# Kernel optimization log

Measured on AMD Instinct MI355X. Metric: run time of the kernel, lower is better.

## Reference

```python
import jax, jax.numpy as jnp
import numpy as np

D = 128          # embed_dim
NB = 30          # hardcoded neighbor count in neighbor_encoder
STEPS = 4        # process_steps
NSYM = 200000    # num_symbols (pad idx = NSYM)
B = 4096         # query batch
FEW = 5          # support pairs


def setup_inputs() -> dict:
    key = jax.random.key(0)
    ks = jax.random.split(key, 32)
    g = lambda i, shape, s=0.02: jax.random.normal(ks[i], shape, dtype=jnp.float32) * s
    inp = {}
    # embedding tables (row NSYM is padding, zeros)
    inp['emb'] = g(0, (NSYM + 1, D), 0.1).at[NSYM].set(0.0)
    inp['emb_var'] = g(1, (NSYM + 1, D), 0.1).at[NSYM].set(0.0)
    # neighbor attention (mean path)
    inp['nW'], inp['nWb'] = g(2, (D, 2 * D)), jnp.zeros((D,), jnp.float32)
    inp['nu'], inp['nub'] = g(3, (1, D)), jnp.zeros((1,), jnp.float32)
    # neighbor attention (var path)
    inp['nvW'], inp['nvWb'] = g(4, (D, 2 * D)), jnp.zeros((D,), jnp.float32)
    inp['nvu'], inp['nvub'] = g(5, (1, D)), jnp.zeros((1,), jnp.float32)
    # SupportEncoder: d_model=2D, d_inner=4D
    inp['p1W'], inp['p1b'] = g(6, (4 * D, 2 * D)), jnp.zeros((4 * D,), jnp.float32)
    inp['p2W'], inp['p2b'] = g(7, (2 * D, 4 * D)), jnp.zeros((2 * D,), jnp.float32)
    inp['ln_a'], inp['ln_b'] = jnp.ones((2 * D,), jnp.float32), jnp.zeros((2 * D,), jnp.float32)
    # QueryEncoder LSTMCell: input 2D, hidden 4D (torch gate order i,f,g,o)
    inp['Wih'], inp['Whh'] = g(8, (16 * D, 2 * D)), g(9, (16 * D, 4 * D))
    inp['bih'], inp['bhh'] = jnp.zeros((16 * D,), jnp.float32), jnp.zeros((16 * D,), jnp.float32)
    # connections: (..., 0)=relation idx, (..., 1)=entity idx
    inp['q_left'] = jax.random.randint(ks[10], (B, NB, 2), 0, NSYM, dtype=jnp.int32)
    inp['q_right'] = jax.random.randint(ks[11], (B, NB, 2), 0, NSYM, dtype=jnp.int32)
    inp['s_left'] = jax.random.randint(ks[12], (FEW, NB, 2), 0, NSYM, dtype=jnp.int32)
    inp['s_right'] = jax.random.randint(ks[13], (FEW, NB, 2), 0, NSYM, dtype=jnp.int32)
    return inp


def _layer_norm(z, a, b, eps=0.001):
    # faithful to torch: std with Bessel correction (ddof=1)
    mu = jnp.mean(z, axis=-1, keepdims=True)
    sigma = jnp.std(z, axis=-1, keepdims=True, ddof=1)
    return (z - mu) / (sigma + eps) * a + b


def reference(emb, emb_var, nW, nWb, nu, nub, nvW, nvWb, nvu, nvub,
              p1W, p1b, p2W, p2b, ln_a, ln_b, Wih, Whh, bih, bhh,
              q_left, q_right, s_left, s_right):

    def neighbor_encoder(conn):
        rel, ent = conn[..., 0], conn[..., 1]
        rel_e, ent_e = emb[rel], emb[ent]                      # [N, NB, D]
        cat = jnp.concatenate([rel_e, ent_e], axis=-1)         # [N, NB, 2D]
        a = jnp.tanh(cat @ nW.T + nWb) @ nu.T + nub            # [N, NB, 1]
        att = jax.nn.softmax(a[..., 0], axis=1)                # softmax over neighbors
        out = jnp.einsum('nk,nkd->nd', att, ent_e)
        rel_v, ent_v = emb_var[rel], emb_var[ent]
        catv = jnp.concatenate([rel_v, ent_v], axis=-1)
        av = jnp.tanh(catv @ nvW.T + nvWb) @ nvu.T + nvub
        attv = jax.nn.softmax(av[..., 0], axis=1)
        out_v = jnp.einsum('nk,nkd->nd', attv, ent_e)          # torch quirk: pools ent_embeds
        return jnp.tanh(out), jnp.tanh(out_v)

    def support_encoder(x):
        h = jax.nn.relu(x @ p1W.T + p1b) @ p2W.T + p2b
        return _layer_norm(h + x, ln_a, ln_b)

    def lstm_cell(x, h, c):
        gates = x @ Wih.T + bih + h @ Whh.T + bhh
        i, f, g_, o = jnp.split(gates, 4, axis=-1)
        c = jax.nn.sigmoid(f) * c + jax.nn.sigmoid(i) * jnp.tanh(g_)
        return jax.nn.sigmoid(o) * jnp.tanh(c), c

    def query_encoder(support, query):
        n = query.shape[0]
        h_r = jnp.zeros((n, 4 * D), query.dtype)
        c = jnp.zeros((n, 4 * D), query.dtype)
        h = query
        for _ in range(STEPS):
            h_r_, c = lstm_cell(query, h_r, c)
            h = query + h_r_[:, :2 * D]
            attn = jax.nn.softmax(h @ support.T, axis=1)
            r = attn @ support
            h_r = jnp.concatenate([h, r], axis=1)
        return h

    ql, qlv = neighbor_encoder(q_left)
    qr, qrv = neighbor_encoder(q_right)
    sl, slv = neighbor_encoder(s_left)
    sr, srv = neighbor_encoder(s_right)

    query = jnp.concatenate([ql, qr], axis=-1)       # [B, 2D]
    query_v = jnp.concatenate([qlv, qrv], axis=-1)
    support = jnp.concatenate([sl, sr], axis=-1)     # [FEW, 2D]
    support_v = jnp.concatenate([slv, srv], axis=-1)

    def match(q, s):
        s_g = support_encoder(s)
        q_g = support_encoder(q)
        q_f = query_encoder(s_g, q_g)
        s_mean = jnp.mean(s_g, axis=0, keepdims=True)  # [1, 2D]
        return (q_f @ s_mean.T)[:, 0]                  # [B]

    score = match(query, support)
    score_var = match(query_v, support_v)
    return jnp.stack([score, score_var])               # [2, B]
```

## Files before the change

kernel.cpp:

```cpp
#include <hip/hip_runtime.h>
#include <math.h>

#define DD    128
#define TWOD  256
#define FOURD 512
#define NBN   30
#define BQ    4096
#define FEWN  5
#define NSYM  200000
#define KTOT  768
#define NGATE 1024
#define ULIVE 256
#define TOTU  (2 * BQ + 2 * FEWN)
#define UPB   4
#define PSTR  136

typedef short bf16x8 __attribute__((ext_vector_type(8)));
typedef float f32x4 __attribute__((ext_vector_type(4)));

__device__ __forceinline__ float sigmoidf_(float x) { return 1.0f / (1.0f + expf(-x)); }

__device__ __forceinline__ float ftanh(float x) {
    float e = __expf(2.0f * x);
    return 1.0f - 2.0f / (e + 1.0f);
}

__device__ __forceinline__ unsigned short f2bf(float f) {
    unsigned int u = __float_as_uint(f);
    unsigned int r = (u + 0x7fffu + ((u >> 16) & 1u)) >> 16;
    return (unsigned short)r;
}

__device__ __forceinline__ float bf2f(unsigned short s) {
    return __uint_as_float(((unsigned int)s) << 16);
}

__device__ __forceinline__ bf16x8 pack8(float4 a, float4 b) {
    union { bf16x8 v; unsigned int u[4]; } r;
    r.u[0] = ((__float_as_uint(a.x) + 0x8000u) >> 16) | ((__float_as_uint(a.y) + 0x8000u) & 0xffff0000u);
    r.u[1] = ((__float_as_uint(a.z) + 0x8000u) >> 16) | ((__float_as_uint(a.w) + 0x8000u) & 0xffff0000u);
    r.u[2] = ((__float_as_uint(b.x) + 0x8000u) >> 16) | ((__float_as_uint(b.y) + 0x8000u) & 0xffff0000u);
    r.u[3] = ((__float_as_uint(b.z) + 0x8000u) >> 16) | ((__float_as_uint(b.w) + 0x8000u) & 0xffff0000u);
    return r.v;
}

__device__ __forceinline__ void gload_lds16(const void* g, void* l) {
    __builtin_amdgcn_global_load_lds((const __attribute__((address_space(1))) unsigned int*)g,
                                     (__attribute__((address_space(3))) unsigned int*)l,
                                     16, 0, 0);
}

__global__ __launch_bounds__(256) void k_prep(
    const float* __restrict__ Wih, const float* __restrict__ Whh,
    const float* __restrict__ bih, const float* __restrict__ bhh,
    const float* __restrict__ p1W, const float* __restrict__ p2W,
    const float* __restrict__ nW, const float* __restrict__ nvW,
    unsigned short* __restrict__ Wbf, float* __restrict__ biasR,
    float* __restrict__ p1WT, float* __restrict__ p2WT,
    unsigned short* __restrict__ Nbf)
{
    int idx = blockIdx.x * 256 + threadIdx.x;
    int stride = gridDim.x * 256;
    for (int i = idx; i < NGATE * KTOT; i += stride) {
        int n = i / KTOT, k = i - n * KTOT;
        int blk = n >> 6, rem = n & 63;
        int g = rem >> 4, ul = rem & 15;
        int u = blk * 16 + ul;
        int srcrow = g * 512 + u;
        float v = (k < TWOD) ? Wih[srcrow * TWOD + k] : Whh[srcrow * FOURD + (k - TWOD)];
        Wbf[i] = f2bf(v);
    }
    for (int n = idx; n < NGATE; n += stride) {
        int blk = n >> 6, rem = n & 63;
        int g = rem >> 4, ul = rem & 15;
        int u = blk * 16 + ul;
        int srcrow = g * 512 + u;
        biasR[n] = bih[srcrow] + bhh[srcrow];
    }
    for (int i = idx; i < FOURD * TWOD; i += stride) {
        int o = i / TWOD, j = i % TWOD;
        p1WT[j * FOURD + o] = p1W[o * TWOD + j];
    }
    for (int i = idx; i < TWOD * FOURD; i += stride) {
        int o = i / FOURD, j = i % FOURD;
        p2WT[j * TWOD + o] = p2W[o * FOURD + j];
    }
    for (int i = idx; i < 2 * DD * TWOD; i += stride) {
        float v = (i < DD * TWOD) ? nW[i] : nvW[i - DD * TWOD];
        Nbf[i] = f2bf(v);
    }
}

__global__ __launch_bounds__(256, 2) void k_neighbor_v4(
    const float* __restrict__ emb, const float* __restrict__ emb_var,
    const unsigned short* __restrict__ Nbf,
    const float* __restrict__ nWb, const float* __restrict__ nu,
    const float* __restrict__ nvWb, const float* __restrict__ nvu,
    const int* __restrict__ q_left, const int* __restrict__ q_right,
    const int* __restrict__ s_left, const int* __restrict__ s_right,
    float* __restrict__ query, float* __restrict__ support)
{
    const int tid  = threadIdx.x;
    const int wave = tid >> 6, lane = tid & 63;
    const int quad = lane >> 4, m15 = lane & 15;
    const int pw   = wave >> 1;
    const int wn   = wave & 1;
    const int u0   = blockIdx.x * UPB;

    __shared__ __align__(16) unsigned short Sg[4 * 32 * PSTR];
    __shared__ int   sidxL[UPB][64];
    __shared__ float aP[2][2][32];
    __shared__ float attL[2][32];

    {
        int un = tid >> 6, i = tid & 63;
        int uu_ = u0 + un; if (uu_ >= TOTU) uu_ = TOTU - 1;
        const int* conn;
        if (uu_ < BQ)                 conn = q_left  + uu_ * (NBN * 2);
        else if (uu_ < 2 * BQ)        conn = q_right + (uu_ - BQ) * (NBN * 2);
        else if (uu_ < 2 * BQ + FEWN) conn = s_left  + (uu_ - 2 * BQ) * (NBN * 2);
        else                          conn = s_right + (uu_ - 2 * BQ - FEWN) * (NBN * 2);
        sidxL[un][i] = (i < NBN * 2) ? conn[i] : NSYM;
    }

    const unsigned short* Bw = Nbf + (size_t)pw * DD * TWOD;
    const float* Wb = pw ? nvWb : nWb;
    const float* uu = pw ? nvu  : nu;
    bf16x8 Bf[4][8];
    float nb[4], un_[4];
#pragma unroll
    for (int t = 0; t < 4; ++t) {
        int n = wn * 64 + t * 16 + m15;
#pragma unroll
        for (int kt = 0; kt < 8; ++kt)
            Bf[t][kt] = *(const bf16x8*)(Bw + n * TWOD + kt * 32 + quad * 8);
        nb[t] = Wb[n];
        un_[t] = uu[n];
    }
    __syncthreads();

    for (int r = 0; r < UPB; ++r) {
        const int uidx = u0 + r;

        {
            const int g = wave;
            const float* table = (g < 2) ? emb : emb_var;
            const int side = g & 1;
            const int colf = (lane & 15) * 8;
            const int rsub = lane >> 4;
#pragma unroll
            for (int i = 0; i < 8; ++i) {
                int row = i * 4 + rsub;
                int sym = sidxL[r][2 * row + side];
                const float* src = table + (size_t)sym * DD + colf;
                float4 x0 = *(const float4*)src;
                float4 x1 = *(const float4*)(src + 4);
                *(bf16x8*)&Sg[(g * 32 + row) * PSTR + colf] = pack8(x0, x1);
            }
        }
        __syncthreads();

        const int pg = pw ? 2 : 0;
        f32x4 acc[2][4] = {};
#pragma unroll
        for (int kt = 0; kt < 8; ++kt) {
            const int g = (kt < 4) ? pg : pg + 1;
            const int coff = (kt & 3) * 32 + quad * 8;
            bf16x8 fa[2];
#pragma unroll
            for (int mt = 0; mt < 2; ++mt)
                fa[mt] = *(const bf16x8*)&Sg[(g * 32 + mt * 16 + m15) * PSTR + coff];
#pragma unroll
            for (int mt = 0; mt < 2; ++mt)
#pragma unroll
                for (int nt = 0; nt < 4; ++nt)
                    acc[mt][nt] = __builtin_amdgcn_mfma_f32_16x16x32_bf16(fa[mt], Bf[nt][kt], acc[mt][nt], 0, 0, 0);
        }

        {
            float part[2][4];
#pragma unroll
            for (int mt = 0; mt < 2; ++mt)
#pragma unroll
                for (int rr = 0; rr < 4; ++rr) {
                    float s = 0.f;
#pragma unroll
                    for (int nt = 0; nt < 4; ++nt)
                        s += un_[nt] * ftanh(acc[mt][nt][rr] + nb[nt]);
                    part[mt][rr] = s;
                }
#pragma unroll
            for (int off = 1; off < 16; off <<= 1)
#pragma unroll
                for (int mt = 0; mt < 2; ++mt)
#pragma unroll
                    for (int rr = 0; rr < 4; ++rr)
                        part[mt][rr] += __shfl_xor(part[mt][rr], off, 64);
            if (m15 == 0) {
#pragma unroll
                for (int mt = 0; mt < 2; ++mt)
#pragma unroll
                    for (int rr = 0; rr < 4; ++rr)
                        aP[pw][wn][mt * 16 + quad * 4 + rr] = part[mt][rr];
            }
        }
        __syncthreads();

        if ((wave & 1) == 0 && lane < 32) {
            const int p = wave >> 1;
            float sc = (lane < NBN) ? aP[p][0][lane] + aP[p][1][lane] : -1e30f;
            float mx = sc;
#pragma unroll
            for (int off = 1; off < 32; off <<= 1) mx = fmaxf(mx, __shfl_xor(mx, off, 64));
            float e = (lane < NBN) ? __expf(sc - mx) : 0.f;
            float sum = e;
#pragma unroll
            for (int off = 1; off < 32; off <<= 1) sum += __shfl_xor(sum, off, 64);
            attL[p][lane] = e / sum;
        }
        __syncthreads();

        {
            const int p = tid >> 7;
            const int d = tid & 127;
            float pool = 0.f;
#pragma unroll
            for (int k = 0; k < NBN; ++k)
                pool += attL[p][k] * bf2f(Sg[(32 + k) * PSTR + d]);
            if (uidx < TOTU) {
                float* dst;
                if (uidx < BQ)                 dst = query   + ((size_t)p * BQ + uidx) * TWOD;
                else if (uidx < 2 * BQ)        dst = query   + ((size_t)p * BQ + (uidx - BQ)) * TWOD + DD;
                else if (uidx < 2 * BQ + FEWN) dst = support + ((size_t)p * FEWN + (uidx - 2 * BQ)) * TWOD;
                else                           dst = support + ((size_t)p * FEWN + (uidx - 2 * BQ - FEWN)) * TWOD + DD;
                dst[d] = ftanh(pool);
            }
        }
        __syncthreads();
    }
}

template <int RPB>
__global__ __launch_bounds__(256) void k_supenc(
    const float* __restrict__ xin, float* __restrict__ xout,
    unsigned short* __restrict__ abf,
    const float* __restrict__ p1WT, const float* __restrict__ p1b,
    const float* __restrict__ p2WT, const float* __restrict__ p2b,
    const float* __restrict__ ln_a, const float* __restrict__ ln_b)
{
    const int tid = threadIdx.x;
    const int r0 = blockIdx.x * RPB;
    __shared__ float X[RPB][TWOD];
    __shared__ float H1[RPB][FOURD];
    __shared__ float red[4][RPB][2];
    __shared__ float muv[RPB], sgv[RPB];

    for (int idx = tid; idx < RPB * TWOD; idx += 256) {
        int r = idx >> 8, j = idx & 255;
        X[r][j] = xin[(size_t)(r0 + r) * TWOD + j];
    }
    __syncthreads();

    {
        float acc[RPB][2] = {};
        for (int j = 0; j < TWOD; j += 4) {
            float w0[4], w1[4];
#pragma unroll
            for (int jj = 0; jj < 4; ++jj) {
                w0[jj] = p1WT[(j + jj) * FOURD + tid];
                w1[jj] = p1WT[(j + jj) * FOURD + tid + 256];
            }
#pragma unroll
            for (int r = 0; r < RPB; ++r) {
                float x[4] __attribute__((aligned(16)));
                *(float4*)x = *(const float4*)&X[r][j];
#pragma unroll
                for (int jj = 0; jj < 4; ++jj) {
                    acc[r][0] += x[jj] * w0[jj];
                    acc[r][1] += x[jj] * w1[jj];
                }
            }
        }
        float b0 = p1b[tid], b1 = p1b[tid + 256];
#pragma unroll
        for (int r = 0; r < RPB; ++r) {
            H1[r][tid]       = fmaxf(acc[r][0] + b0, 0.f);
            H1[r][tid + 256] = fmaxf(acc[r][1] + b1, 0.f);
        }
    }
    __syncthreads();

    float z[RPB];
    {
        float acc[RPB] = {};
        for (int j = 0; j < FOURD; j += 4) {
            float w[4];
#pragma unroll
            for (int jj = 0; jj < 4; ++jj) w[jj] = p2WT[(j + jj) * TWOD + tid];
#pragma unroll
            for (int r = 0; r < RPB; ++r) {
                float h[4] __attribute__((aligned(16)));
                *(float4*)h = *(const float4*)&H1[r][j];
#pragma unroll
                for (int jj = 0; jj < 4; ++jj) acc[r] += h[jj] * w[jj];
            }
        }
        float b = p2b[tid];
#pragma unroll
        for (int r = 0; r < RPB; ++r) z[r] = acc[r] + b + X[r][tid];
    }
    {
        float s[RPB], ss[RPB];
#pragma unroll
        for (int r = 0; r < RPB; ++r) { s[r] = z[r]; ss[r] = z[r] * z[r]; }
#pragma unroll
        for (int off = 1; off < 64; off <<= 1)
#pragma unroll
            for (int r = 0; r < RPB; ++r) {
                s[r]  += __shfl_xor(s[r],  off, 64);
                ss[r] += __shfl_xor(ss[r], off, 64);
            }
        const int wv = tid >> 6, lane = tid & 63;
        if (lane == 0) {
#pragma unroll
            for (int r = 0; r < RPB; ++r) { red[wv][r][0] = s[r]; red[wv][r][1] = ss[r]; }
        }
        __syncthreads();
        if (tid < RPB) {
            float st  = red[0][tid][0] + red[1][tid][0] + red[2][tid][0] + red[3][tid][0];
            float sst = red[0][tid][1] + red[1][tid][1] + red[2][tid][1] + red[3][tid][1];
            float mu  = st / (float)TWOD;
            float var = fmaxf((sst - (float)TWOD * mu * mu) / ((float)TWOD - 1.f), 0.f);
            muv[tid] = mu; sgv[tid] = sqrtf(var);
        }
        __syncthreads();
    }
#pragma unroll
    for (int r = 0; r < RPB; ++r) {
        float o = (z[r] - muv[r]) / (sgv[r] + 1e-3f) * ln_a[tid] + ln_b[tid];
        xout[(size_t)(r0 + r) * TWOD + tid] = o;
        if (abf) abf[(size_t)(r0 + r) * KTOT + tid] = f2bf(o);
    }
}

__global__ __launch_bounds__(256) void k_lstm_mfma(
    const unsigned short* __restrict__ Abf,
    const unsigned short* __restrict__ Wbf,
    const float* __restrict__ biasR,
    float* __restrict__ cst, float* __restrict__ hbuf)
{
    __shared__ __align__(16) unsigned short As[128 * 32];
    __shared__ __align__(16) unsigned short Bs[128 * 32];
    const int tid  = threadIdx.x;
    const int wave = tid >> 6, lane = tid & 63;
    const int quad = lane >> 4, m15 = lane & 15;
    const int m0 = blockIdx.x * 128;
    const int n0 = blockIdx.y * 128;
    const int wm = wave >> 1, wn = wave & 1;
    const int lrow = lane >> 2, lslot = lane & 3;

    f32x4 acc[4][4] = {};

    for (int kt = 0; kt < KTOT / 32; ++kt) {
        const int k0 = kt * 32;
        __syncthreads();
#pragma unroll
        for (int t = 0; t < 2; ++t) {
            int c = wave * 2 + t;
            int row = c * 16 + lrow;
            int kg = lslot ^ ((row >> 1) & 3);
            gload_lds16(Abf + (size_t)(m0 + row) * KTOT + k0 + kg * 8, As + c * 512);
            gload_lds16(Wbf + (size_t)(n0 + row) * KTOT + k0 + kg * 8, Bs + c * 512);
        }
        __syncthreads();

        bf16x8 fa[4], fb[4];
#pragma unroll
        for (int mi = 0; mi < 4; ++mi) {
            int ra = wm * 64 + mi * 16 + m15;
            int sa = quad ^ ((ra >> 1) & 3);
            fa[mi] = *(const bf16x8*)(As + ra * 32 + sa * 8);
            int rb = wn * 64 + mi * 16 + m15;
            int sb = quad ^ ((rb >> 1) & 3);
            fb[mi] = *(const bf16x8*)(Bs + rb * 32 + sb * 8);
        }
#pragma unroll
        for (int mi = 0; mi < 4; ++mi)
#pragma unroll
            for (int ni = 0; ni < 4; ++ni)
                acc[mi][ni] = __builtin_amdgcn_mfma_f32_16x16x32_bf16(fa[mi], fb[ni], acc[mi][ni], 0, 0, 0);
    }

    const int u = ((n0 + wn * 64) >> 2) + m15;
    float bg[4];
#pragma unroll
    for (int g = 0; g < 4; ++g) bg[g] = biasR[n0 + wn * 64 + g * 16 + m15];
#pragma unroll
    for (int mi = 0; mi < 4; ++mi) {
#pragma unroll
        for (int r = 0; r < 4; ++r) {
            int gm = m0 + wm * 64 + mi * 16 + quad * 4 + r;
            size_t cidx = (size_t)gm * ULIVE + u;
            float pi = acc[mi][0][r] + bg[0];
            float pf = acc[mi][1][r] + bg[1];
            float pg = acc[mi][2][r] + bg[2];
            float po = acc[mi][3][r] + bg[3];
            float cn = sigmoidf_(pf) * cst[cidx] + sigmoidf_(pi) * tanhf(pg);
            cst[cidx]  = cn;
            hbuf[cidx] = sigmoidf_(po) * tanhf(cn);
        }
    }
}

__global__ __launch_bounds__(256) void k_lstm_attn(
    const float* __restrict__ qg, const float* __restrict__ hbuf,
    const float* __restrict__ sg, unsigned short* __restrict__ Abf,
    float* __restrict__ hfin)
{
    const int tid = threadIdx.x;
    const int p   = blockIdx.y;
    const int wv = tid >> 6, lane = tid & 63;
    __shared__ float sgl[FEWN][TWOD];
    for (int idx = tid; idx < FEWN * TWOD; idx += 256)
        sgl[idx >> 8][idx & 255] = sg[p * FEWN * TWOD + idx];
    __syncthreads();
    const int j0 = lane * 4;
    for (int rr = 0; rr < 8; ++rr) {
        int row = blockIdx.x * 32 + wv * 8 + rr;
        size_t g = (size_t)p * BQ + row;
        float4 q4 = *(const float4*)(qg + g * TWOD + j0);
        float4 t4 = *(const float4*)(hbuf + g * ULIVE + j0);
        float h[4] __attribute__((aligned(16))) = {q4.x + t4.x, q4.y + t4.y, q4.z + t4.z, q4.w + t4.w};
        float sv[FEWN][4] __attribute__((aligned(16)));
        float pa[FEWN];
#pragma unroll
        for (int f = 0; f < FEWN; ++f) {
            *(float4*)sv[f] = *(const float4*)&sgl[f][j0];
            pa[f] = h[0] * sv[f][0] + h[1] * sv[f][1] + h[2] * sv[f][2] + h[3] * sv[f][3];
        }
#pragma unroll
        for (int off = 1; off < 64; off <<= 1)
#pragma unroll
            for (int f = 0; f < FEWN; ++f) pa[f] += __shfl_xor(pa[f], off, 64);
        float mx = pa[0];
#pragma unroll
        for (int f = 1; f < FEWN; ++f) mx = fmaxf(mx, pa[f]);
        float sum = 0.f, e[FEWN];
#pragma unroll
        for (int f = 0; f < FEWN; ++f) { e[f] = expf(pa[f] - mx); sum += e[f]; }
        float inv = 1.f / sum;
        float r4[4] __attribute__((aligned(16))) = {0.f, 0.f, 0.f, 0.f};
#pragma unroll
        for (int f = 0; f < FEWN; ++f) {
            float a = e[f] * inv;
#pragma unroll
            for (int q = 0; q < 4; ++q) r4[q] += a * sv[f][q];
        }
        unsigned short tb[4] __attribute__((aligned(8)));
#pragma unroll
        for (int q = 0; q < 4; ++q) tb[q] = f2bf(h[q]);
        *(uint2*)(Abf + g * KTOT + TWOD + j0) = *(uint2*)tb;
#pragma unroll
        for (int q = 0; q < 4; ++q) tb[q] = f2bf(r4[q]);
        *(uint2*)(Abf + g * KTOT + FOURD + j0) = *(uint2*)tb;
        *(float4*)(hfin + g * TWOD + j0) = *(float4*)h;
    }
}

__global__ __launch_bounds__(256) void k_score(
    const float* __restrict__ hfin, const float* __restrict__ sg, float* __restrict__ out)
{
    const int tid = threadIdx.x;
    const int p   = blockIdx.y;
    __shared__ float sm[TWOD];
    if (tid < TWOD) {
        const float* s = sg + p * FEWN * TWOD + tid;
        sm[tid] = (s[0] + s[TWOD] + s[2 * TWOD] + s[3 * TWOD] + s[4 * TWOD]) / 5.0f;
    }
    __syncthreads();
    const int wv = tid >> 6, lane = tid & 63;
    const int j0 = lane * 4;
    for (int rr = 0; rr < 8; ++rr) {
        int row = blockIdx.x * 32 + wv * 8 + rr;
        const float* h = hfin + ((size_t)p * BQ + row) * TWOD + j0;
        float4 h4 = *(const float4*)h;
        float4 s4 = *(const float4*)&sm[j0];
        float pv = h4.x * s4.x + h4.y * s4.y + h4.z * s4.z + h4.w * s4.w;
#pragma unroll
        for (int off = 1; off < 64; off <<= 1) pv += __shfl_xor(pv, off, 64);
        if (lane == 0) out[p * BQ + row] = pv;
    }
}

extern "C" void kernel_launch(void* const* d_in, const int* in_sizes, int n_in,
                              void* d_out, int out_size, void* d_ws, size_t ws_size,
                              hipStream_t stream)
{
    const float* emb     = (const float*)d_in[0];
    const float* emb_var = (const float*)d_in[1];
    const float* nW      = (const float*)d_in[2];
    const float* nWb     = (const float*)d_in[3];
    const float* nu      = (const float*)d_in[4];
    const float* nub     = (const float*)d_in[5];
    const float* nvW     = (const float*)d_in[6];
    const float* nvWb    = (const float*)d_in[7];
    const float* nvu     = (const float*)d_in[8];
    const float* nvub    = (const float*)d_in[9];
    const float* p1W     = (const float*)d_in[10];
    const float* p1b     = (const float*)d_in[11];
    const float* p2W     = (const float*)d_in[12];
    const float* p2b     = (const float*)d_in[13];
    const float* ln_a    = (const float*)d_in[14];
    const float* ln_b    = (const float*)d_in[15];
    const float* Wih     = (const float*)d_in[16];
    const float* Whh     = (const float*)d_in[17];
    const float* bih     = (const float*)d_in[18];
    const float* bhh     = (const float*)d_in[19];
    const int* q_left    = (const int*)d_in[20];
    const int* q_right   = (const int*)d_in[21];
    const int* s_left    = (const int*)d_in[22];
    const int* s_right   = (const int*)d_in[23];

    float* ws = (float*)d_ws;
    size_t o = 0;
    float* p1WT     = ws + o; o += FOURD * TWOD;
    float* p2WT     = ws + o; o += FOURD * TWOD;
    float* biasR    = ws + o; o += NGATE;
    float* query    = ws + o; o += (size_t)2 * BQ * TWOD;
    float* supportB = ws + o; o += 2 * FEWN * TWOD;
    float* qg       = ws + o; o += (size_t)2 * BQ * TWOD;
    float* sg       = ws + o; o += 2 * FEWN * TWOD;
    float* cst      = ws + o; o += (size_t)2 * BQ * ULIVE;
    float* hbuf     = ws + o; o += (size_t)2 * BQ * ULIVE;
    unsigned short* Wbf = (unsigned short*)(ws + o); o += (size_t)NGATE * KTOT / 2;
    unsigned short* Abf = (unsigned short*)(ws + o); o += (size_t)2 * BQ * KTOT / 2;
    unsigned short* Nbf = (unsigned short*)(ws + o); o += (size_t)2 * DD * TWOD / 2;
    float* hfin     = query;

    hipMemsetAsync(cst, 0, (size_t)2 * BQ * ULIVE * sizeof(float), stream);
    hipMemsetAsync(Abf, 0, (size_t)2 * BQ * KTOT * sizeof(unsigned short), stream);

    k_prep<<<dim3(1024), dim3(256), 0, stream>>>(Wih, Whh, bih, bhh, p1W, p2W, nW, nvW,
                                                 Wbf, biasR, p1WT, p2WT, Nbf);
    k_neighbor_v4<<<dim3((TOTU + UPB - 1) / UPB), dim3(256), 0, stream>>>(
        emb, emb_var, Nbf, nWb, nu, nvWb, nvu,
        q_left, q_right, s_left, s_right, query, supportB);
    k_supenc<8><<<dim3(2 * BQ / 8), dim3(256), 0, stream>>>(query, qg, Abf, p1WT, p1b, p2WT, p2b, ln_a, ln_b);
    k_supenc<1><<<dim3(2 * FEWN), dim3(256), 0, stream>>>(supportB, sg, (unsigned short*)nullptr,
                                                          p1WT, p1b, p2WT, p2b, ln_a, ln_b);
    for (int s = 0; s < 4; ++s) {
        k_lstm_mfma<<<dim3(2 * BQ / 128, NGATE / 128), dim3(256), 0, stream>>>(Abf, Wbf, biasR, cst, hbuf);
        k_lstm_attn<<<dim3(BQ / 32, 2), dim3(256), 0, stream>>>(qg, hbuf, sg, Abf, hfin);
    }
    k_score<<<dim3(BQ / 32, 2), dim3(256), 0, stream>>>(hfin, sg, (float*)d_out);
}
```

Before: 607.6 us.

## Gather neighbor embeddings straight to LDS in fp32; skip zero hidden-state K in first LSTM step

```diff
diff --git a/kernel.cpp b/kernel.cpp
--- a/kernel.cpp
+++ b/kernel.cpp
@@ -13,7 +13,6 @@
 #define ULIVE 256
 #define TOTU  (2 * BQ + 2 * FEWN)
 #define UPB   4
-#define PSTR  136
 
 typedef short bf16x8 __attribute__((ext_vector_type(8)));
 typedef float f32x4 __attribute__((ext_vector_type(4)));
@@ -29,10 +28,6 @@
     unsigned int u = __float_as_uint(f);
     unsigned int r = (u + 0x7fffu + ((u >> 16) & 1u)) >> 16;
     return (unsigned short)r;
-}
-
-__device__ __forceinline__ float bf2f(unsigned short s) {
-    return __uint_as_float(((unsigned int)s) << 16);
 }
 
 __device__ __forceinline__ bf16x8 pack8(float4 a, float4 b) {
@@ -91,7 +86,7 @@
     }
 }
 
-__global__ __launch_bounds__(256, 2) void k_neighbor_v4(
+__global__ __launch_bounds__(256, 2) void k_neighbor_v5(
     const float* __restrict__ emb, const float* __restrict__ emb_var,
     const unsigned short* __restrict__ Nbf,
     const float* __restrict__ nWb, const float* __restrict__ nu,
@@ -107,7 +102,7 @@
     const int wn   = wave & 1;
     const int u0   = blockIdx.x * UPB;
 
-    __shared__ __align__(16) unsigned short Sg[4 * 32 * PSTR];
+    __shared__ __align__(16) float Sgf[4 * 32 * DD];
     __shared__ int   sidxL[UPB][64];
     __shared__ float aP[2][2][32];
     __shared__ float attL[2][32];
@@ -146,16 +141,14 @@
             const int g = wave;
             const float* table = (g < 2) ? emb : emb_var;
             const int side = g & 1;
-            const int colf = (lane & 15) * 8;
-            const int rsub = lane >> 4;
-#pragma unroll
-            for (int i = 0; i < 8; ++i) {
-                int row = i * 4 + rsub;
-                int sym = sidxL[r][2 * row + side];
-                const float* src = table + (size_t)sym * DD + colf;
-                float4 x0 = *(const float4*)src;
-                float4 x1 = *(const float4*)(src + 4);
-                *(bf16x8*)&Sg[(g * 32 + row) * PSTR + colf] = pack8(x0, x1);
+            const int rl = lane >> 5;
+            const int cb = lane & 31;
+#pragma unroll
+            for (int i = 0; i < 16; ++i) {
+                const int row = 2 * i + rl;
+                const int sym = sidxL[r][2 * row + side];
+                const float* src = table + (size_t)sym * DD + ((cb ^ (row & 7)) << 2);
+                gload_lds16(src, &Sgf[(g * 32 + 2 * i) * DD]);
             }
         }
         __syncthreads();
@@ -165,11 +158,17 @@
 #pragma unroll
         for (int kt = 0; kt < 8; ++kt) {
             const int g = (kt < 4) ? pg : pg + 1;
-            const int coff = (kt & 3) * 32 + quad * 8;
+            const int cb0 = (kt & 3) * 8 + quad * 2;
             bf16x8 fa[2];
 #pragma unroll
-            for (int mt = 0; mt < 2; ++mt)
-                fa[mt] = *(const bf16x8*)&Sg[(g * 32 + mt * 16 + m15) * PSTR + coff];
+            for (int mt = 0; mt < 2; ++mt) {
+                const int row = mt * 16 + m15;
+                const float* rp = &Sgf[(g * 32 + row) * DD];
+                const int s = row & 7;
+                float4 x0 = *(const float4*)(rp + ((cb0 ^ s) << 2));
+                float4 x1 = *(const float4*)(rp + (((cb0 + 1) ^ s) << 2));
+                fa[mt] = pack8(x0, x1);
+            }
 #pragma unroll
             for (int mt = 0; mt < 2; ++mt)
 #pragma unroll
@@ -223,10 +222,11 @@
         {
             const int p = tid >> 7;
             const int d = tid & 127;
+            const int cbp = d >> 2, ofs = d & 3;
             float pool = 0.f;
 #pragma unroll
             for (int k = 0; k < NBN; ++k)
-                pool += attL[p][k] * bf2f(Sg[(32 + k) * PSTR + d]);
+                pool += attL[p][k] * Sgf[(32 + k) * DD + ((cbp ^ (k & 7)) << 2) + ofs];
             if (uidx < TOTU) {
                 float* dst;
                 if (uidx < BQ)                 dst = query   + ((size_t)p * BQ + uidx) * TWOD;
@@ -347,7 +347,8 @@
     const unsigned short* __restrict__ Abf,
     const unsigned short* __restrict__ Wbf,
     const float* __restrict__ biasR,
-    float* __restrict__ cst, float* __restrict__ hbuf)
+    float* __restrict__ cst, float* __restrict__ hbuf,
+    const int nkt)
 {
     __shared__ __align__(16) unsigned short As[128 * 32];
     __shared__ __align__(16) unsigned short Bs[128 * 32];
@@ -361,7 +362,7 @@
 
     f32x4 acc[4][4] = {};
 
-    for (int kt = 0; kt < KTOT / 32; ++kt) {
+    for (int kt = 0; kt < nkt; ++kt) {
         const int k0 = kt * 32;
         __syncthreads();
 #pragma unroll
@@ -538,18 +539,18 @@
     float* hfin     = query;
 
     hipMemsetAsync(cst, 0, (size_t)2 * BQ * ULIVE * sizeof(float), stream);
-    hipMemsetAsync(Abf, 0, (size_t)2 * BQ * KTOT * sizeof(unsigned short), stream);
 
     k_prep<<<dim3(1024), dim3(256), 0, stream>>>(Wih, Whh, bih, bhh, p1W, p2W, nW, nvW,
                                                  Wbf, biasR, p1WT, p2WT, Nbf);
-    k_neighbor_v4<<<dim3((TOTU + UPB - 1) / UPB), dim3(256), 0, stream>>>(
+    k_neighbor_v5<<<dim3((TOTU + UPB - 1) / UPB), dim3(256), 0, stream>>>(
         emb, emb_var, Nbf, nWb, nu, nvWb, nvu,
         q_left, q_right, s_left, s_right, query, supportB);
     k_supenc<8><<<dim3(2 * BQ / 8), dim3(256), 0, stream>>>(query, qg, Abf, p1WT, p1b, p2WT, p2b, ln_a, ln_b);
     k_supenc<1><<<dim3(2 * FEWN), dim3(256), 0, stream>>>(supportB, sg, (unsigned short*)nullptr,
                                                           p1WT, p1b, p2WT, p2b, ln_a, ln_b);
     for (int s = 0; s < 4; ++s) {
-        k_lstm_mfma<<<dim3(2 * BQ / 128, NGATE / 128), dim3(256), 0, stream>>>(Abf, Wbf, biasR, cst, hbuf);
+        k_lstm_mfma<<<dim3(2 * BQ / 128, NGATE / 128), dim3(256), 0, stream>>>(
+            Abf, Wbf, biasR, cst, hbuf, s == 0 ? TWOD / 32 : KTOT / 32);
         k_lstm_attn<<<dim3(BQ / 32, 2), dim3(256), 0, stream>>>(qg, hbuf, sg, Abf, hfin);
     }
     k_score<<<dim3(BQ / 32, 2), dim3(256), 0, stream>>>(hfin, sg, (float*)d_out);
```

Measured after the change: 616.3 us. No clear change (+1.4%).

## Double-buffer LSTM GEMM with 64-wide K steps and skip zero hidden state

Applied to the files above, without the earlier changes.

```diff
diff --git a/kernel.cpp b/kernel.cpp
--- a/kernel.cpp
+++ b/kernel.cpp
@@ -347,10 +347,11 @@
     const unsigned short* __restrict__ Abf,
     const unsigned short* __restrict__ Wbf,
     const float* __restrict__ biasR,
-    float* __restrict__ cst, float* __restrict__ hbuf)
-{
-    __shared__ __align__(16) unsigned short As[128 * 32];
-    __shared__ __align__(16) unsigned short Bs[128 * 32];
+    float* __restrict__ cst, float* __restrict__ hbuf,
+    const int nkt)
+{
+    __shared__ __align__(16) unsigned short As[2 * 2 * 4096];
+    __shared__ __align__(16) unsigned short Bs[2 * 2 * 4096];
     const int tid  = threadIdx.x;
     const int wave = tid >> 6, lane = tid & 63;
     const int quad = lane >> 4, m15 = lane & 15;
@@ -361,34 +362,54 @@
 
     f32x4 acc[4][4] = {};
 
-    for (int kt = 0; kt < KTOT / 32; ++kt) {
-        const int k0 = kt * 32;
-        __syncthreads();
+    auto stage = [&](int buf, int k0) {
 #pragma unroll
         for (int t = 0; t < 2; ++t) {
-            int c = wave * 2 + t;
-            int row = c * 16 + lrow;
-            int kg = lslot ^ ((row >> 1) & 3);
-            gload_lds16(Abf + (size_t)(m0 + row) * KTOT + k0 + kg * 8, As + c * 512);
-            gload_lds16(Wbf + (size_t)(n0 + row) * KTOT + k0 + kg * 8, Bs + c * 512);
-        }
-        __syncthreads();
-
-        bf16x8 fa[4], fb[4];
-#pragma unroll
-        for (int mi = 0; mi < 4; ++mi) {
-            int ra = wm * 64 + mi * 16 + m15;
-            int sa = quad ^ ((ra >> 1) & 3);
-            fa[mi] = *(const bf16x8*)(As + ra * 32 + sa * 8);
-            int rb = wn * 64 + mi * 16 + m15;
-            int sb = quad ^ ((rb >> 1) & 3);
-            fb[mi] = *(const bf16x8*)(Bs + rb * 32 + sb * 8);
-        }
-#pragma unroll
-        for (int mi = 0; mi < 4; ++mi)
-#pragma unroll
-            for (int ni = 0; ni < 4; ++ni)
-                acc[mi][ni] = __builtin_amdgcn_mfma_f32_16x16x32_bf16(fa[mi], fb[ni], acc[mi][ni], 0, 0, 0);
+            const int c = wave * 2 + t;
+            const int row = c * 16 + lrow;
+            const int kg = lslot ^ ((row >> 1) & 3);
+#pragma unroll
+            for (int kh = 0; kh < 2; ++kh) {
+                gload_lds16(Abf + (size_t)(m0 + row) * KTOT + k0 + kh * 32 + kg * 8,
+                            As + buf * 8192 + kh * 4096 + c * 512);
+                gload_lds16(Wbf + (size_t)(n0 + row) * KTOT + k0 + kh * 32 + kg * 8,
+                            Bs + buf * 8192 + kh * 4096 + c * 512);
+            }
+        }
+    };
+
+    auto compute = [&](int buf) {
+#pragma unroll
+        for (int kh = 0; kh < 2; ++kh) {
+            const unsigned short* pA = As + buf * 8192 + kh * 4096;
+            const unsigned short* pB = Bs + buf * 8192 + kh * 4096;
+            bf16x8 fa[4], fb[4];
+#pragma unroll
+            for (int mi = 0; mi < 4; ++mi) {
+                int ra = wm * 64 + mi * 16 + m15;
+                int sa = quad ^ ((ra >> 1) & 3);
+                fa[mi] = *(const bf16x8*)(pA + ra * 32 + sa * 8);
+                int rb = wn * 64 + mi * 16 + m15;
+                int sb = quad ^ ((rb >> 1) & 3);
+                fb[mi] = *(const bf16x8*)(pB + rb * 32 + sb * 8);
+            }
+#pragma unroll
+            for (int mi = 0; mi < 4; ++mi)
+#pragma unroll
+                for (int ni = 0; ni < 4; ++ni)
+                    acc[mi][ni] = __builtin_amdgcn_mfma_f32_16x16x32_bf16(fa[mi], fb[ni], acc[mi][ni], 0, 0, 0);
+        }
+    };
+
+    stage(0, 0);
+    __syncthreads();
+
+    int cur = 0;
+    for (int kt = 0; kt < nkt; ++kt) {
+        if (kt + 1 < nkt) stage(cur ^ 1, (kt + 1) * 64);
+        compute(cur);
+        __syncthreads();
+        cur ^= 1;
     }
 
     const int u = ((n0 + wn * 64) >> 2) + m15;
@@ -538,7 +559,6 @@
     float* hfin     = query;
 
     hipMemsetAsync(cst, 0, (size_t)2 * BQ * ULIVE * sizeof(float), stream);
-    hipMemsetAsync(Abf, 0, (size_t)2 * BQ * KTOT * sizeof(unsigned short), stream);
 
     k_prep<<<dim3(1024), dim3(256), 0, stream>>>(Wih, Whh, bih, bhh, p1W, p2W, nW, nvW,
                                                  Wbf, biasR, p1WT, p2WT, Nbf);
@@ -549,7 +569,8 @@
     k_supenc<1><<<dim3(2 * FEWN), dim3(256), 0, stream>>>(supportB, sg, (unsigned short*)nullptr,
                                                           p1WT, p1b, p2WT, p2b, ln_a, ln_b);
     for (int s = 0; s < 4; ++s) {
-        k_lstm_mfma<<<dim3(2 * BQ / 128, NGATE / 128), dim3(256), 0, stream>>>(Abf, Wbf, biasR, cst, hbuf);
+        k_lstm_mfma<<<dim3(2 * BQ / 128, NGATE / 128), dim3(256), 0, stream>>>(
+            Abf, Wbf, biasR, cst, hbuf, s == 0 ? TWOD / 64 : KTOT / 64);
         k_lstm_attn<<<dim3(BQ / 32, 2), dim3(256), 0, stream>>>(qg, hbuf, sg, Abf, hfin);
     }
     k_score<<<dim3(BQ / 32, 2), dim3(256), 0, stream>>>(hfin, sg, (float*)d_out);
```

New measurement: 590.0 us. -2.9%, faster.
